# Performance work log

Measured on AMD Instinct MI355X. Metric: run time of the kernel, lower is better.

Reference implementation:

```python
import jax, jax.numpy as jnp
import numpy as np

H = 12  # num_heads

def _alibi_bias(num_heads, n, dtype):
    # slopes: ratio**i for i in 1..H, ratio = 2**(-8/H)
    ratio = 2.0 ** (-8.0 / num_heads)
    slopes = ratio ** jnp.arange(1, num_heads + 1, dtype=jnp.float32)  # [H]
    pos = jnp.arange(n)
    rel = jnp.abs(pos[None, :] - pos[:, None]).astype(jnp.float32)  # [N,N]
    return (-slopes[:, None, None] * rel[None]).astype(dtype)  # [H,N,N]

def setup_inputs() -> dict:
    key = jax.random.key(0)
    ks = jax.random.split(key, 5)
    B, N, C = 16, 1024, 768
    s = 0.02
    return {
        "x": jax.random.normal(ks[0], (B, N, C), jnp.float32),
        "w_qkv": jax.random.normal(ks[1], (3 * C, C), jnp.float32) * s,
        "b_qkv": jax.random.normal(ks[2], (3 * C,), jnp.float32) * s,
        "w_proj": jax.random.normal(ks[3], (C, C), jnp.float32) * s,
        "b_proj": jax.random.normal(ks[4], (C,), jnp.float32) * s,
    }

def reference(x, w_qkv, b_qkv, w_proj, b_proj):
    B, N, C = x.shape
    D = C // H
    scale = D ** -0.5
    qkv = x @ w_qkv.T + b_qkv                       # [B,N,3C]
    qkv = qkv.reshape(B, N, 3, H, D)
    q = qkv[:, :, 0].transpose(0, 2, 1, 3)          # [B,H,N,D]
    k = qkv[:, :, 1].transpose(0, 2, 1, 3)
    v = qkv[:, :, 2].transpose(0, 2, 1, 3)
    bias = _alibi_bias(H, N, x.dtype)               # [H,N,N]
    scores = jnp.einsum('bhnd,bhmd->bhnm', q, k) * scale + bias[None]
    attn = jax.nn.softmax(scores, axis=-1)
    out = jnp.einsum('bhnm,bhmd->bhnd', attn, v)    # [B,H,N,D]
    out = out.transpose(0, 2, 1, 3).reshape(B, N, C)
    return out @ w_proj.T + b_proj
```

## Files before the change

### kernel.cpp

```cpp
#include <hip/hip_runtime.h>


typedef unsigned short u16;
typedef unsigned int u32;
typedef __attribute__((ext_vector_type(8))) short short8;
typedef __attribute__((ext_vector_type(4))) float f32x4;

__device__ __forceinline__ u16 f2bf(float f) {
    u32 u = __float_as_uint(f);
    u32 r = u + 0x7FFFu + ((u >> 16) & 1u);
    return (u16)(r >> 16);
}

__device__ __forceinline__ f32x4 mfma16(short8 a, short8 b, f32x4 c) {
    return __builtin_amdgcn_mfma_f32_16x16x32_bf16(a, b, c, 0, 0, 0);
}
__device__ __forceinline__ u32 cvtpk_bf16(float lo, float hi) {
    u32 r;
    asm("v_cvt_pk_bf16_f32 %0, %1, %2" : "=v"(r) : "v"(lo), "v"(hi));
    return r;
}

typedef __attribute__((address_space(1))) const unsigned int gu32_t;
typedef __attribute__((address_space(3))) unsigned int su32_t;
__device__ __forceinline__ void gl16(const u16* g, u16* s) {
    __builtin_amdgcn_global_load_lds((gu32_t*)g, (su32_t*)s, 16, 0, 0);
}

__global__ void cvt_all(const float* __restrict__ x, const float* __restrict__ wq,
                        const float* __restrict__ wp, u16* __restrict__ Xb,
                        u16* __restrict__ Wqkvb, u16* __restrict__ Wprojb) {
    int i = blockIdx.x * blockDim.x + threadIdx.x;
    int stride = gridDim.x * blockDim.x;
    for (int idx = i; idx < 3735552; idx += stride) {
        const float* src;
        u16* dst;
        int k;
        if (idx < 3145728) { src = x; dst = Xb; k = idx; }
        else if (idx < 3588096) { src = wq; dst = Wqkvb; k = idx - 3145728; }
        else { src = wp; dst = Wprojb; k = idx - 3588096; }
        float4 v = *(const float4*)(src + (size_t)k * 4);
        ushort4 o;
        o.x = f2bf(v.x); o.y = f2bf(v.y); o.z = f2bf(v.z); o.w = f2bf(v.w);
        *(ushort4*)(dst + (size_t)k * 4) = o;
    }
}

template <int EPI>
__global__ __launch_bounds__(256) void gemm_nt(
    const u16* __restrict__ A, const u16* __restrict__ Bw,
    const float* __restrict__ bias, u16* __restrict__ outb, float* __restrict__ outf,
    int nTilesN)
{
    constexpr int K = 768;
    constexpr int nkt = K / 32;
    __shared__ __align__(16) u16 lA[3][128 * 32];
    __shared__ __align__(16) u16 lB[3][128 * 32];

    int tid = threadIdx.x;
    int bid = blockIdx.x;
    int nwg = gridDim.x;
    int cpx = nwg >> 3;
    int swz = (bid & 7) * cpx + (bid >> 3);
    int bm = swz / nTilesN;
    int bn = swz - bm * nTilesN;
    int m0 = bm * 128, n0 = bn * 128;

    int sr = tid >> 2;
    int sc = (tid & 3) << 3;
    const u16* pA = A + (size_t)(m0 + sr) * K + sc;
    const u16* pB = Bw + (size_t)(n0 + sr) * K + sc;
    int lo = tid * 8;

    gl16(pA, &lA[0][lo]);
    gl16(pA + (size_t)64 * K, &lA[0][lo + 2048]);
    gl16(pB, &lB[0][lo]);
    gl16(pB + (size_t)64 * K, &lB[0][lo + 2048]);
    gl16(pA + 32, &lA[1][lo]);
    gl16(pA + (size_t)64 * K + 32, &lA[1][lo + 2048]);
    gl16(pB + 32, &lB[1][lo]);
    gl16(pB + (size_t)64 * K + 32, &lB[1][lo + 2048]);

    int w = tid >> 6, lane = tid & 63;
    int wr = (w >> 1) << 6, wc = (w & 1) << 6;
    int fq = lane >> 4, fr = lane & 15;
    f32x4 acc[4][4] = {};

    for (int kt = 0; kt < nkt; ++kt) {
        int cur = kt % 3;
        if (kt < nkt - 1) { asm volatile("s_waitcnt vmcnt(4)" ::: "memory"); }
        else              { asm volatile("s_waitcnt vmcnt(0)" ::: "memory"); }
        __builtin_amdgcn_sched_barrier(0);
        __builtin_amdgcn_s_barrier();
        __builtin_amdgcn_sched_barrier(0);
        if (kt + 2 < nkt) {
            int nx = (kt + 2) % 3;
            const u16* qA = pA + (kt + 2) * 32;
            const u16* qB = pB + (kt + 2) * 32;
            gl16(qA, &lA[nx][lo]);
            gl16(qA + (size_t)64 * K, &lA[nx][lo + 2048]);
            gl16(qB, &lB[nx][lo]);
            gl16(qB + (size_t)64 * K, &lB[nx][lo + 2048]);
        }
        short8 af[4], bfr[4];
#pragma unroll
        for (int i = 0; i < 4; ++i)
            af[i] = *(const short8*)&lA[cur][(wr + i * 16 + fr) * 32 + fq * 8];
#pragma unroll
        for (int j = 0; j < 4; ++j)
            bfr[j] = *(const short8*)&lB[cur][(wc + j * 16 + fr) * 32 + fq * 8];
        __builtin_amdgcn_s_setprio(1);
#pragma unroll
        for (int i = 0; i < 4; ++i)
#pragma unroll
            for (int j = 0; j < 4; ++j)
                acc[i][j] = mfma16(af[i], bfr[j], acc[i][j]);
        __builtin_amdgcn_s_setprio(0);
    }

    if (EPI == 0) {
        int nbase = n0 + wc;
        int s = nbase / 768;
        int hh = (nbase % 768) >> 6;
        int b = m0 >> 10;
        int i0 = (m0 & 1023) + wr;
        u16* obase = outb + (((size_t)s * 16 + b) * 12 + hh) * 1024 * 64;
#pragma unroll
        for (int j = 0; j < 4; ++j) {
            float bval = bias[nbase + j * 16 + fr];
            int d = j * 16 + fr;
#pragma unroll
            for (int i = 0; i < 4; ++i) {
                int r0 = i0 + i * 16 + fq * 4;
#pragma unroll
                for (int r = 0; r < 4; ++r)
                    obase[(size_t)(r0 + r) * 64 + d] = f2bf(acc[i][j][r] + bval);
            }
        }
    } else {
#pragma unroll
        for (int j = 0; j < 4; ++j) {
            int col = n0 + wc + j * 16 + fr;
            float bval = bias[col];
#pragma unroll
            for (int i = 0; i < 4; ++i) {
                int row0 = m0 + wr + i * 16 + fq * 4;
#pragma unroll
                for (int r = 0; r < 4; ++r)
                    outf[(size_t)(row0 + r) * 768 + col] = acc[i][j][r] + bval;
            }
        }
    }
}

__global__ __launch_bounds__(256) void attn_alibi(
    const u16* __restrict__ QKV, u16* __restrict__ att)
{
    int g = blockIdx.x;
    int xcd = g & 7;
    int idx = g >> 3;
    int qt = idx & 15;
    int bh = xcd * 24 + (idx >> 4);
    int h = bh % 12;
    int b = bh / 12;
    int q0 = qt * 64;
    const u16* Qg = QKV + (size_t)bh * 65536;
    const u16* Kg = QKV + (size_t)(192 + bh) * 65536;
    const u16* Vg = QKV + (size_t)(384 + bh) * 65536;

    __shared__ __align__(16) u16 Qs[64][72];
    __shared__ __align__(16) u16 Ks[64][72];
    __shared__ __align__(16) u16 Vt[64][72];
    __shared__ __align__(16) u16 Ps[64][72];

    int tid = threadIdx.x, w = tid >> 6, lane = tid & 63;
    int fq = lane >> 4, fr = lane & 15;

    for (int c = tid; c < 512; c += 256) {
        int r = c >> 3, d = (c & 7) * 8;
        *(uint4*)&Qs[r][d] = *(const uint4*)(Qg + (size_t)(q0 + r) * 64 + d);
    }
    __syncthreads();
    short8 aq0 = *(const short8*)&Qs[w * 16 + fr][fq * 8];
    short8 aq1 = *(const short8*)&Qs[w * 16 + fr][32 + fq * 8];

    const float C1 = 0.125f * 1.44269504f;
    float c2 = __builtin_amdgcn_exp2f(-(2.0f / 3.0f) * (float)(h + 1)) * 1.44269504f;
    int distThr = (int)(40.0f / c2);
    int lo_kv = q0 - 63 - distThr;
    int hi_kv = q0 + 63 + distThr;
    int t_lo = (lo_kv <= 0) ? 0 : (lo_kv >> 6);
    int t_hi = (hi_kv >= 1023) ? 15 : (hi_kv >> 6);

    int sr0 = tid >> 3;
    int sr1 = sr0 + 32;
    int vk0 = sr0 * 2;
    int sc = (tid & 7) * 8;
    int vswz = (tid & 7) << 3;

    uint4 kr0 = *(const uint4*)(Kg + (size_t)(t_lo * 64 + sr0) * 64 + sc);
    uint4 kr1 = *(const uint4*)(Kg + (size_t)(t_lo * 64 + sr1) * 64 + sc);
    uint4 vr0 = *(const uint4*)(Vg + (size_t)(t_lo * 64 + vk0) * 64 + sc);
    uint4 vr1 = *(const uint4*)(Vg + (size_t)(t_lo * 64 + vk0 + 1) * 64 + sc);

    float di = (float)(q0 + w * 16 + fr - fq * 4);
    float lsum = 0.f;
    f32x4 acc[4] = {};

    for (int it = t_lo; it <= t_hi; ++it) {
        __syncthreads();
        *(uint4*)&Ks[sr0][sc] = kr0;
        *(uint4*)&Ks[sr1][sc] = kr1;
        {
            const u16* v0 = (const u16*)&vr0;
            const u16* v1 = (const u16*)&vr1;
            int col = vk0 ^ vswz;
#pragma unroll
            for (int jj = 0; jj < 8; ++jj)
                *(u32*)&Vt[sc + jj][col] = (u32)v0[jj] | ((u32)v1[jj] << 16);
        }
        __syncthreads();

        if (it < t_hi) {
            int kvn = (it + 1) * 64;
            kr0 = *(const uint4*)(Kg + (size_t)(kvn + sr0) * 64 + sc);
            kr1 = *(const uint4*)(Kg + (size_t)(kvn + sr1) * 64 + sc);
            vr0 = *(const uint4*)(Vg + (size_t)(kvn + vk0) * 64 + sc);
            vr1 = *(const uint4*)(Vg + (size_t)(kvn + vk0 + 1) * 64 + sc);
        }

        f32x4 sfr[4];
        __builtin_amdgcn_s_setprio(1);
#pragma unroll
        for (int ct = 0; ct < 4; ++ct) {
            short8 bk0 = *(const short8*)&Ks[ct * 16 + fr][fq * 8];
            short8 bk1 = *(const short8*)&Ks[ct * 16 + fr][32 + fq * 8];
            f32x4 s0 = {0.f, 0.f, 0.f, 0.f};
            s0 = mfma16(bk0, aq0, s0);
            s0 = mfma16(bk1, aq1, s0);
            sfr[ct] = s0;
        }
        __builtin_amdgcn_s_setprio(0);

        float dkv = di - (float)(it * 64);
#pragma unroll
        for (int ct = 0; ct < 4; ++ct) {
            float t0 = dkv - (float)(ct * 16);
            float e0 = __builtin_amdgcn_exp2f(fmaf(sfr[ct][0], C1, -c2 * fabsf(t0)));
            float e1 = __builtin_amdgcn_exp2f(fmaf(sfr[ct][1], C1, -c2 * fabsf(t0 - 1.0f)));
            float e2 = __builtin_amdgcn_exp2f(fmaf(sfr[ct][2], C1, -c2 * fabsf(t0 - 2.0f)));
            float e3 = __builtin_amdgcn_exp2f(fmaf(sfr[ct][3], C1, -c2 * fabsf(t0 - 3.0f)));
            lsum += (e0 + e1) + (e2 + e3);
            uint2 pk;
            pk.x = cvtpk_bf16(e0, e1);
            pk.y = cvtpk_bf16(e2, e3);
            *(uint2*)&Ps[w * 16 + fr][ct * 16 + fq * 4] = pk;
        }

        short8 pa0 = *(const short8*)&Ps[w * 16 + fr][fq * 8];
        short8 pa1 = *(const short8*)&Ps[w * 16 + fr][32 + fq * 8];
        __builtin_amdgcn_s_setprio(1);
#pragma unroll
        for (int dt = 0; dt < 4; ++dt) {
            int row = dt * 16 + fr;
            int swzr = (row >> 3) << 3;
            short8 bv0 = *(const short8*)&Vt[row][(fq * 8) ^ swzr];
            short8 bv1 = *(const short8*)&Vt[row][(32 + fq * 8) ^ swzr];
            acc[dt] = mfma16(pa0, bv0, acc[dt]);
            acc[dt] = mfma16(pa1, bv1, acc[dt]);
        }
        __builtin_amdgcn_s_setprio(0);
    }

    float l = lsum;
    l += __shfl_xor(l, 16);
    l += __shfl_xor(l, 32);
    float rlo = 1.0f / l;
    float rl[4];
#pragma unroll
    for (int r = 0; r < 4; ++r)
        rl[r] = __shfl(rlo, fq * 4 + r);

#pragma unroll
    for (int dt = 0; dt < 4; ++dt)
#pragma unroll
        for (int r = 0; r < 4; ++r) {
            int ig = q0 + w * 16 + fq * 4 + r;
            att[((size_t)(b * 1024 + ig) * 12 + h) * 64 + dt * 16 + fr] =
                (u16)cvtpk_bf16(acc[dt][r] * rl[r], 0.f);
        }
}

extern "C" void kernel_launch(void* const* d_in, const int* in_sizes, int n_in,
                              void* d_out, int out_size, void* d_ws, size_t ws_size,
                              hipStream_t stream) {
    const float* x      = (const float*)d_in[0];
    const float* w_qkv  = (const float*)d_in[1];
    const float* b_qkv  = (const float*)d_in[2];
    const float* w_proj = (const float*)d_in[3];
    const float* b_proj = (const float*)d_in[4];
    float* out = (float*)d_out;

    char* ws = (char*)d_ws;
    u16* Xb     = (u16*)ws;
    u16* Wqkvb  = (u16*)(ws + 25165824);
    u16* Wprojb = (u16*)(ws + 28704768);
    u16* QKVb   = (u16*)(ws + 29884416);
    u16* Attb   = Xb;

    cvt_all<<<2048, 256, 0, stream>>>(x, w_qkv, w_proj, Xb, Wqkvb, Wprojb);

    gemm_nt<0><<<128 * 18, 256, 0, stream>>>(Xb, Wqkvb, b_qkv, QKVb, nullptr, 18);
    attn_alibi<<<3072, 256, 0, stream>>>(QKVb, Attb);
    gemm_nt<1><<<128 * 6, 256, 0, stream>>>(Attb, Wprojb, b_proj, nullptr, out, 6);
}
```

Measured before the change: 197.8 us.

## Use 512-thread GEMM blocks with 2x4 warp layout; load Q fragments directly

The GEMM now runs 8 waves per 128x128 tile instead of 4. Each wave computes a 64x32 sub-tile, and each thread issues one global-to-LDS load per operand per k-step instead of two, with the vmcnt waits adjusted to match. The epilogue recomputes head and column offsets per 16-column group. In attention, Q fragments are read straight from global memory, which drops the Qs LDS staging and one __syncthreads. The aim is more waves for latency hiding and lower LDS use, at the cost of more LDS fragment reads of A per MFMA.

```diff
diff --git a/kernel.cpp b/kernel.cpp
--- a/kernel.cpp
+++ b/kernel.cpp
@@ -47,7 +47,7 @@
 }
 
 template <int EPI>
-__global__ __launch_bounds__(256) void gemm_nt(
+__global__ __launch_bounds__(512) void gemm_nt(
     const u16* __restrict__ A, const u16* __restrict__ Bw,
     const float* __restrict__ bias, u16* __restrict__ outb, float* __restrict__ outf,
     int nTilesN)
@@ -72,79 +72,72 @@
     const u16* pB = Bw + (size_t)(n0 + sr) * K + sc;
     int lo = tid * 8;
 
-    gl16(pA, &lA[0][lo]);
-    gl16(pA + (size_t)64 * K, &lA[0][lo + 2048]);
-    gl16(pB, &lB[0][lo]);
-    gl16(pB + (size_t)64 * K, &lB[0][lo + 2048]);
+    gl16(pA,      &lA[0][lo]);
+    gl16(pB,      &lB[0][lo]);
     gl16(pA + 32, &lA[1][lo]);
-    gl16(pA + (size_t)64 * K + 32, &lA[1][lo + 2048]);
     gl16(pB + 32, &lB[1][lo]);
-    gl16(pB + (size_t)64 * K + 32, &lB[1][lo + 2048]);
 
     int w = tid >> 6, lane = tid & 63;
-    int wr = (w >> 1) << 6, wc = (w & 1) << 6;
+    int wm = w >> 2, wn = w & 3;
     int fq = lane >> 4, fr = lane & 15;
-    f32x4 acc[4][4] = {};
+    f32x4 acc[4][2] = {};
 
     for (int kt = 0; kt < nkt; ++kt) {
         int cur = kt % 3;
-        if (kt < nkt - 1) { asm volatile("s_waitcnt vmcnt(4)" ::: "memory"); }
+        if (kt < nkt - 1) { asm volatile("s_waitcnt vmcnt(2)" ::: "memory"); }
         else              { asm volatile("s_waitcnt vmcnt(0)" ::: "memory"); }
         __builtin_amdgcn_sched_barrier(0);
         __builtin_amdgcn_s_barrier();
         __builtin_amdgcn_sched_barrier(0);
         if (kt + 2 < nkt) {
             int nx = (kt + 2) % 3;
-            const u16* qA = pA + (kt + 2) * 32;
-            const u16* qB = pB + (kt + 2) * 32;
-            gl16(qA, &lA[nx][lo]);
-            gl16(qA + (size_t)64 * K, &lA[nx][lo + 2048]);
-            gl16(qB, &lB[nx][lo]);
-            gl16(qB + (size_t)64 * K, &lB[nx][lo + 2048]);
-        }
-        short8 af[4], bfr[4];
+            gl16(pA + (kt + 2) * 32, &lA[nx][lo]);
+            gl16(pB + (kt + 2) * 32, &lB[nx][lo]);
+        }
+        short8 af[4], bfr[2];
 #pragma unroll
         for (int i = 0; i < 4; ++i)
-            af[i] = *(const short8*)&lA[cur][(wr + i * 16 + fr) * 32 + fq * 8];
-#pragma unroll
-        for (int j = 0; j < 4; ++j)
-            bfr[j] = *(const short8*)&lB[cur][(wc + j * 16 + fr) * 32 + fq * 8];
+            af[i] = *(const short8*)&lA[cur][(wm * 64 + i * 16 + fr) * 32 + fq * 8];
+#pragma unroll
+        for (int j = 0; j < 2; ++j)
+            bfr[j] = *(const short8*)&lB[cur][(wn * 32 + j * 16 + fr) * 32 + fq * 8];
         __builtin_amdgcn_s_setprio(1);
 #pragma unroll
         for (int i = 0; i < 4; ++i)
 #pragma unroll
-            for (int j = 0; j < 4; ++j)
+            for (int j = 0; j < 2; ++j)
                 acc[i][j] = mfma16(af[i], bfr[j], acc[i][j]);
         __builtin_amdgcn_s_setprio(0);
     }
 
     if (EPI == 0) {
-        int nbase = n0 + wc;
-        int s = nbase / 768;
-        int hh = (nbase % 768) >> 6;
         int b = m0 >> 10;
-        int i0 = (m0 & 1023) + wr;
-        u16* obase = outb + (((size_t)s * 16 + b) * 12 + hh) * 1024 * 64;
-#pragma unroll
-        for (int j = 0; j < 4; ++j) {
-            float bval = bias[nbase + j * 16 + fr];
-            int d = j * 16 + fr;
+        int i0 = (m0 & 1023) + wm * 64;
+#pragma unroll
+        for (int j = 0; j < 2; ++j) {
+            int colb = n0 + wn * 32 + j * 16;
+            int s = colb / 768;
+            int rem = colb % 768;
+            int hh = rem >> 6;
+            int d0 = rem & 63;
+            float bval = bias[colb + fr];
+            u16* obase = outb + (((size_t)s * 16 + b) * 12 + hh) * 65536;
 #pragma unroll
             for (int i = 0; i < 4; ++i) {
                 int r0 = i0 + i * 16 + fq * 4;
 #pragma unroll
                 for (int r = 0; r < 4; ++r)
-                    obase[(size_t)(r0 + r) * 64 + d] = f2bf(acc[i][j][r] + bval);
+                    obase[(size_t)(r0 + r) * 64 + d0 + fr] = f2bf(acc[i][j][r] + bval);
             }
         }
     } else {
 #pragma unroll
-        for (int j = 0; j < 4; ++j) {
-            int col = n0 + wc + j * 16 + fr;
+        for (int j = 0; j < 2; ++j) {
+            int col = n0 + wn * 32 + j * 16 + fr;
             float bval = bias[col];
 #pragma unroll
             for (int i = 0; i < 4; ++i) {
-                int row0 = m0 + wr + i * 16 + fq * 4;
+                int row0 = m0 + wm * 64 + i * 16 + fq * 4;
 #pragma unroll
                 for (int r = 0; r < 4; ++r)
                     outf[(size_t)(row0 + r) * 768 + col] = acc[i][j][r] + bval;
@@ -168,7 +161,6 @@
     const u16* Kg = QKV + (size_t)(192 + bh) * 65536;
     const u16* Vg = QKV + (size_t)(384 + bh) * 65536;
 
-    __shared__ __align__(16) u16 Qs[64][72];
     __shared__ __align__(16) u16 Ks[64][72];
     __shared__ __align__(16) u16 Vt[64][72];
     __shared__ __align__(16) u16 Ps[64][72];
@@ -176,13 +168,8 @@
     int tid = threadIdx.x, w = tid >> 6, lane = tid & 63;
     int fq = lane >> 4, fr = lane & 15;
 
-    for (int c = tid; c < 512; c += 256) {
-        int r = c >> 3, d = (c & 7) * 8;
-        *(uint4*)&Qs[r][d] = *(const uint4*)(Qg + (size_t)(q0 + r) * 64 + d);
-    }
-    __syncthreads();
-    short8 aq0 = *(const short8*)&Qs[w * 16 + fr][fq * 8];
-    short8 aq1 = *(const short8*)&Qs[w * 16 + fr][32 + fq * 8];
+    short8 aq0 = *(const short8*)(Qg + (size_t)(q0 + w * 16 + fr) * 64 + fq * 8);
+    short8 aq1 = *(const short8*)(Qg + (size_t)(q0 + w * 16 + fr) * 64 + 32 + fq * 8);
 
     const float C1 = 0.125f * 1.44269504f;
     float c2 = __builtin_amdgcn_exp2f(-(2.0f / 3.0f) * (float)(h + 1)) * 1.44269504f;
@@ -310,7 +297,7 @@
 
     cvt_all<<<2048, 256, 0, stream>>>(x, w_qkv, w_proj, Xb, Wqkvb, Wprojb);
 
-    gemm_nt<0><<<128 * 18, 256, 0, stream>>>(Xb, Wqkvb, b_qkv, QKVb, nullptr, 18);
+    gemm_nt<0><<<128 * 18, 512, 0, stream>>>(Xb, Wqkvb, b_qkv, QKVb, nullptr, 18);
     attn_alibi<<<3072, 256, 0, stream>>>(QKVb, Attb);
-    gemm_nt<1><<<128 * 6, 256, 0, stream>>>(Attb, Wprojb, b_proj, nullptr, out, 6);
-}
+    gemm_nt<1><<<128 * 6, 512, 0, stream>>>(Attb, Wprojb, b_proj, nullptr, out, 6);
+}
```

Result: faster. 193.3 us (-2.3%).
